# Kernel tuning notes

Measured on AMD Instinct MI355X. Metric: run time of the kernel, lower is better.

Reference implementation:

```python
import jax, jax.numpy as jnp
import numpy as np

N = 50000
E = 800000
IN, HID, OUT = 256, 128, 64
NEG_SLOPE = 0.2


def _gat(x, src, dst, W, a_src, a_dst, b, heads, dim, concat):
    # PyG GATConv (eval mode, self-loops already appended to src/dst)
    xh = (x @ W).reshape(N, heads, dim)              # [N,H,D]
    s_src = jnp.einsum('nhd,hd->nh', xh, a_src)       # [N,H]
    s_dst = jnp.einsum('nhd,hd->nh', xh, a_dst)
    e = jax.nn.leaky_relu(s_src[src] + s_dst[dst], NEG_SLOPE)  # [Etot,H]
    m = jax.ops.segment_max(e, dst, num_segments=N)
    e = jnp.exp(e - m[dst])
    z = jax.ops.segment_sum(e, dst, num_segments=N)
    alpha = e / z[dst]                                # segment softmax over incoming edges
    msg = xh[src] * alpha[:, :, None]                 # [Etot,H,D] gather + weight
    out = jax.ops.segment_sum(msg, dst, num_segments=N)  # scatter-add aggregate
    out = out.reshape(N, heads * dim) if concat else out.mean(axis=1)
    return out + b


def setup_inputs():
    key = jax.random.key(0)
    ks = jax.random.split(key, 20)
    sc = 0.05
    inp = {
        'x': jax.random.normal(ks[0], (N, IN), jnp.float32),
        'edge_index': jax.random.randint(ks[1], (2, E), 0, N, jnp.int64) if jax.config.read('jax_enable_x64') else jax.random.randint(ks[1], (2, E), 0, N, jnp.int32),
        # semantic MLP
        'w1': jax.random.normal(ks[2], (IN, HID), jnp.float32) * sc,
        'b1': jnp.zeros((HID,), jnp.float32),
        'w2': jax.random.normal(ks[3], (HID, HID), jnp.float32) * sc,
        'b2': jnp.zeros((HID,), jnp.float32),
        # gat1: HID -> HID//2, heads=4, concat -> 2*HID
        'g1_w': jax.random.normal(ks[4], (HID, 4 * (HID // 2)), jnp.float32) * sc,
        'g1_asrc': jax.random.normal(ks[5], (4, HID // 2), jnp.float32) * sc,
        'g1_adst': jax.random.normal(ks[6], (4, HID // 2), jnp.float32) * sc,
        'g1_b': jnp.zeros((2 * HID,), jnp.float32),
        # gat2: 2*HID -> OUT, heads=2, mean
        'g2_w': jax.random.normal(ks[7], (2 * HID, 2 * OUT), jnp.float32) * sc,
        'g2_asrc': jax.random.normal(ks[8], (2, OUT), jnp.float32) * sc,
        'g2_adst': jax.random.normal(ks[9], (2, OUT), jnp.float32) * sc,
        'g2_b': jnp.zeros((OUT,), jnp.float32),
        # gat3: OUT -> OUT, heads=1, mean
        'g3_w': jax.random.normal(ks[10], (OUT, OUT), jnp.float32) * sc,
        'g3_asrc': jax.random.normal(ks[11], (1, OUT), jnp.float32) * sc,
        'g3_adst': jax.random.normal(ks[12], (1, OUT), jnp.float32) * sc,
        'g3_b': jnp.zeros((OUT,), jnp.float32),
    }
    return inp


def reference(x, edge_index, w1, b1, w2, b2,
              g1_w, g1_asrc, g1_adst, g1_b,
              g2_w, g2_asrc, g2_adst, g2_b,
              g3_w, g3_asrc, g3_adst, g3_b):
    # add self loops once (PyG GATConv default add_self_loops=True)
    loop = jnp.arange(N, dtype=edge_index.dtype)
    src = jnp.concatenate([edge_index[0], loop])
    dst = jnp.concatenate([edge_index[1], loop])
    # semantic MLP (eval: dropout is identity)
    h = jax.nn.relu(x @ w1 + b1)
    h = jax.nn.relu(h @ w2 + b2)
    h = jax.nn.elu(_gat(h, src, dst, g1_w, g1_asrc, g1_adst, g1_b, 4, HID // 2, True))
    h = jax.nn.elu(_gat(h, src, dst, g2_w, g2_asrc, g2_adst, g2_b, 2, OUT, False))
    h = _gat(h, src, dst, g3_w, g3_asrc, g3_adst, g3_b, 1, OUT, False)
    return h
```

## Files before the change

kernel.cpp:

```cpp
#include <hip/hip_runtime.h>
#include <hip/hip_fp16.h>
#include <math.h>

#define NN 50000
#define NE 800000

static inline int ceil_div_h(int a, int b) { return (a + b - 1) / b; }

typedef _Float16 half8 __attribute__((ext_vector_type(8)));
typedef float f32x4 __attribute__((ext_vector_type(4)));

__global__ __launch_bounds__(256)
void prep_kernel(const float* __restrict__ w1, const float* __restrict__ w2,
                 const float* __restrict__ g1w, const float* __restrict__ g2w,
                 const float* __restrict__ g3w, __half* __restrict__ wt,
                 int* __restrict__ cursor) {
  int idx = blockIdx.x * 256 + threadIdx.x;
  if (idx < NN) cursor[idx] = 0;
  const float* W; int K, N, li;
  if (idx < 32768)        { W = w1;  K = 256; N = 128; li = idx; }
  else if (idx < 49152)   { W = w2;  K = 128; N = 128; li = idx - 32768; }
  else if (idx < 81920)   { W = g1w; K = 128; N = 256; li = idx - 49152; }
  else if (idx < 114688)  { W = g2w; K = 256; N = 128; li = idx - 81920; }
  else if (idx < 118784)  { W = g3w; K = 64;  N = 64;  li = idx - 114688; }
  else return;
  int n = li / K, k = li - n * K;
  wt[idx] = __float2half_rn(W[(size_t)k * N + n]);
}

__global__ __launch_bounds__(256)
void mlp_gat1_fused(const float* __restrict__ x,
                    const __half* __restrict__ wt1,
                    const float* __restrict__ b1,
                    const __half* __restrict__ wt2,
                    const float* __restrict__ b2,
                    const __half* __restrict__ wtg1,
                    const float* __restrict__ a_src, const float* __restrict__ a_dst,
                    __half* __restrict__ xh1,
                    float* __restrict__ s_src, float* __restrict__ s_dst) {
  constexpr int SA = 40;
  constexpr int SH = 136;
  __shared__ __align__(16) _Float16 smem[25088];
  _Float16* As   = smem;
  _Float16* Bs12 = smem + 2560;
  _Float16* h1s  = smem + 7680;
  _Float16* h2s  = smem + 16384;
  _Float16* Bs3  = Bs12;
  const int tid = threadIdx.x;
  const int bm = blockIdx.x * 64;
  const int wave = tid >> 6, lane = tid & 63;
  const int l16 = lane & 15, quad = lane >> 4;
  const int wm = (wave & 1) * 32;
  const int wn = (wave >> 1) * 64;

  {
    f32x4 acc[2][4] = {};
    for (int k0 = 0; k0 < 256; k0 += 32) {
      #pragma unroll
      for (int i = 0; i < 2; ++i) {
        int idx = tid + i * 256;
        int m = idx >> 3, q = idx & 7;
        int gm = bm + m;
        float4 v = make_float4(0.f, 0.f, 0.f, 0.f);
        if (gm < NN) v = *(const float4*)&x[(size_t)gm * 256 + k0 + q * 4];
        union { __half2 h2[2]; float2 f2; } u;
        u.h2[0] = __floats2half2_rn(v.x, v.y);
        u.h2[1] = __floats2half2_rn(v.z, v.w);
        *(float2*)&As[m * SA + q * 4] = u.f2;
      }
      #pragma unroll
      for (int i = 0; i < 2; ++i) {
        int idx = tid + i * 256;
        int n = idx >> 2, kq = (idx & 3) * 8;
        *(float4*)&Bs12[n * SA + kq] = *(const float4*)&wt1[(size_t)n * 256 + k0 + kq];
      }
      __syncthreads();
      half8 af[2], bf[4];
      #pragma unroll
      for (int mi = 0; mi < 2; ++mi)
        af[mi] = *(const half8*)&As[(wm + mi * 16 + l16) * SA + quad * 8];
      #pragma unroll
      for (int ni = 0; ni < 4; ++ni)
        bf[ni] = *(const half8*)&Bs12[(wn + ni * 16 + l16) * SA + quad * 8];
      #pragma unroll
      for (int mi = 0; mi < 2; ++mi)
        #pragma unroll
        for (int ni = 0; ni < 4; ++ni)
          acc[mi][ni] = __builtin_amdgcn_mfma_f32_16x16x32_f16(af[mi], bf[ni], acc[mi][ni], 0, 0, 0);
      __syncthreads();
    }
    #pragma unroll
    for (int mi = 0; mi < 2; ++mi)
      #pragma unroll
      for (int r = 0; r < 4; ++r) {
        int row = wm + mi * 16 + quad * 4 + r;
        #pragma unroll
        for (int ni = 0; ni < 4; ++ni) {
          int col = wn + ni * 16 + l16;
          float v = acc[mi][ni][r] + b1[col];
          v = fmaxf(v, 0.f);
          h1s[row * SH + col] = (_Float16)v;
        }
      }
  }
  __syncthreads();

  {
    f32x4 acc[2][4] = {};
    for (int k0 = 0; k0 < 128; k0 += 32) {
      #pragma unroll
      for (int i = 0; i < 2; ++i) {
        int idx = tid + i * 256;
        int n = idx >> 2, kq = (idx & 3) * 8;
        *(float4*)&Bs12[n * SA + kq] = *(const float4*)&wt2[(size_t)n * 128 + k0 + kq];
      }
      __syncthreads();
      half8 af[2], bf[4];
      #pragma unroll
      for (int mi = 0; mi < 2; ++mi)
        af[mi] = *(const half8*)&h1s[(wm + mi * 16 + l16) * SH + k0 + quad * 8];
      #pragma unroll
      for (int ni = 0; ni < 4; ++ni)
        bf[ni] = *(const half8*)&Bs12[(wn + ni * 16 + l16) * SA + quad * 8];
      #pragma unroll
      for (int mi = 0; mi < 2; ++mi)
        #pragma unroll
        for (int ni = 0; ni < 4; ++ni)
          acc[mi][ni] = __builtin_amdgcn_mfma_f32_16x16x32_f16(af[mi], bf[ni], acc[mi][ni], 0, 0, 0);
      __syncthreads();
    }
    #pragma unroll
    for (int mi = 0; mi < 2; ++mi)
      #pragma unroll
      for (int r = 0; r < 4; ++r) {
        int row = wm + mi * 16 + quad * 4 + r;
        #pragma unroll
        for (int ni = 0; ni < 4; ++ni) {
          int col = wn + ni * 16 + l16;
          float v = acc[mi][ni][r] + b2[col];
          v = fmaxf(v, 0.f);
          h2s[row * SH + col] = (_Float16)v;
        }
      }
  }
  __syncthreads();

  {
    f32x4 acc[4][4] = {};
    const int wn3 = wave * 64;
    for (int k0 = 0; k0 < 128; k0 += 32) {
      #pragma unroll
      for (int i = 0; i < 4; ++i) {
        int idx = tid + i * 256;
        int n = idx >> 2, kq = (idx & 3) * 8;
        *(float4*)&Bs3[n * SA + kq] = *(const float4*)&wtg1[(size_t)n * 128 + k0 + kq];
      }
      __syncthreads();
      half8 af[4], bf[4];
      #pragma unroll
      for (int mi = 0; mi < 4; ++mi)
        af[mi] = *(const half8*)&h2s[(mi * 16 + l16) * SH + k0 + quad * 8];
      #pragma unroll
      for (int ni = 0; ni < 4; ++ni)
        bf[ni] = *(const half8*)&Bs3[(wn3 + ni * 16 + l16) * SA + quad * 8];
      #pragma unroll
      for (int mi = 0; mi < 4; ++mi)
        #pragma unroll
        for (int ni = 0; ni < 4; ++ni)
          acc[mi][ni] = __builtin_amdgcn_mfma_f32_16x16x32_f16(af[mi], bf[ni], acc[mi][ni], 0, 0, 0);
      __syncthreads();
    }
    float asv[4], adv[4];
    #pragma unroll
    for (int ni = 0; ni < 4; ++ni) {
      int d = ni * 16 + l16;
      asv[ni] = a_src[wave * 64 + d];
      adv[ni] = a_dst[wave * 64 + d];
    }
    #pragma unroll
    for (int mi = 0; mi < 4; ++mi) {
      #pragma unroll
      for (int r = 0; r < 4; ++r) {
        int gm = bm + mi * 16 + quad * 4 + r;
        float ss = 0.f, sd = 0.f;
        #pragma unroll
        for (int ni = 0; ni < 4; ++ni) {
          float v = acc[mi][ni][r];
          ss = fmaf(v, asv[ni], ss);
          sd = fmaf(v, adv[ni], sd);
          if (gm < NN) xh1[(size_t)gm * 256 + wn3 + ni * 16 + l16] = __float2half_rn(v);
        }
        #pragma unroll
        for (int off = 1; off < 16; off <<= 1) {
          ss += __shfl_xor(ss, off, 64);
          sd += __shfl_xor(sd, off, 64);
        }
        if (l16 == 0 && gm < NN) {
          s_src[gm * 4 + wave] = ss;
          s_dst[gm * 4 + wave] = sd;
        }
      }
    }
  }
}

template<int BM, int TN, int WR, int WC, int ACT, int OUTH, int AF32, int HS>
__global__ __launch_bounds__(256)
void mfma_gemm(const void* __restrict__ Av, const __half* __restrict__ Bt,
               const float* __restrict__ bias, void* __restrict__ Cv,
               const float* __restrict__ a_src, const float* __restrict__ a_dst,
               float* __restrict__ s_src, float* __restrict__ s_dst,
               int M, int N, int K) {
  constexpr int FM = BM / WR / 16;
  constexpr int FN = TN / WC / 16;
  constexpr int SA = 40;
  __shared__ __align__(16) _Float16 As[BM * SA];
  __shared__ __align__(16) _Float16 Bs[TN * SA];
  const int tid = threadIdx.x;
  const int bm = blockIdx.y * BM, bn = blockIdx.x * TN;
  const int wave = tid >> 6, lane = tid & 63;
  const int wm = (wave % WR) * (BM / WR);
  const int wn = (wave / WR) * (TN / WC);
  const int l16 = lane & 15, quad = lane >> 4;

  f32x4 acc[FM][FN] = {};

  for (int k0 = 0; k0 < K; k0 += 32) {
    if (AF32) {
      const float* A = (const float*)Av;
      #pragma unroll
      for (int i = 0; i < (BM * 8) / 256; ++i) {
        int idx = tid + i * 256;
        int m = idx >> 3, q = idx & 7;
        int gm = bm + m;
        float4 v = make_float4(0.f, 0.f, 0.f, 0.f);
        if (gm < M) v = *(const float4*)&A[(size_t)gm * K + k0 + q * 4];
        union { __half2 h2[2]; float2 f2; } u;
        u.h2[0] = __floats2half2_rn(v.x, v.y);
        u.h2[1] = __floats2half2_rn(v.z, v.w);
        *(float2*)&As[m * SA + q * 4] = u.f2;
      }
    } else {
      const __half* A = (const __half*)Av;
      #pragma unroll
      for (int i = 0; i < (BM * 4) / 256; ++i) {
        int idx = tid + i * 256;
        int m = idx >> 2, q = (idx & 3) * 8;
        int gm = bm + m;
        float4 raw = make_float4(0.f, 0.f, 0.f, 0.f);
        if (gm < M) raw = *(const float4*)&A[(size_t)gm * K + k0 + q];
        *(float4*)&As[m * SA + q] = raw;
      }
    }
    #pragma unroll
    for (int i = 0; i < (TN * 4) / 256; ++i) {
      int idx = tid + i * 256;
      int n = idx >> 2, kq = (idx & 3) * 8;
      float4 raw = *(const float4*)&Bt[(size_t)(bn + n) * K + k0 + kq];
      *(float4*)&Bs[n * SA + kq] = raw;
    }
    __syncthreads();
    half8 af[FM], bf[FN];
    #pragma unroll
    for (int mi = 0; mi < FM; ++mi)
      af[mi] = *(const half8*)&As[(wm + mi * 16 + l16) * SA + quad * 8];
    #pragma unroll
    for (int ni = 0; ni < FN; ++ni)
      bf[ni] = *(const half8*)&Bs[(wn + ni * 16 + l16) * SA + quad * 8];
    #pragma unroll
    for (int mi = 0; mi < FM; ++mi)
      #pragma unroll
      for (int ni = 0; ni < FN; ++ni)
        acc[mi][ni] = __builtin_amdgcn_mfma_f32_16x16x32_f16(af[mi], bf[ni], acc[mi][ni], 0, 0, 0);
    __syncthreads();
  }

  #pragma unroll
  for (int mi = 0; mi < FM; ++mi) {
    #pragma unroll
    for (int r = 0; r < 4; ++r) {
      int gm = bm + wm + mi * 16 + quad * 4 + r;
      if (gm >= M) continue;
      #pragma unroll
      for (int ni = 0; ni < FN; ++ni) {
        int gn = bn + wn + ni * 16 + l16;
        float v = acc[mi][ni][r];
        if (bias) v += bias[gn];
        if (ACT == 1) v = fmaxf(v, 0.f);
        if (OUTH) ((__half*)Cv)[(size_t)gm * N + gn] = __float2half_rn(v);
        else      ((float*)Cv)[(size_t)gm * N + gn] = v;
      }
    }
  }

  if (HS > 0) {
    const int h = (bn + wn) >> 6;
    float asv[FN], adv[FN];
    #pragma unroll
    for (int ni = 0; ni < FN; ++ni) {
      int d = ni * 16 + l16;
      asv[ni] = a_src[h * 64 + d];
      adv[ni] = a_dst[h * 64 + d];
    }
    #pragma unroll
    for (int mi = 0; mi < FM; ++mi) {
      #pragma unroll
      for (int r = 0; r < 4; ++r) {
        float ss = 0.f, sd = 0.f;
        #pragma unroll
        for (int ni = 0; ni < FN; ++ni) {
          float v = acc[mi][ni][r];
          ss = fmaf(v, asv[ni], ss);
          sd = fmaf(v, adv[ni], sd);
        }
        #pragma unroll
        for (int off = 1; off < 16; off <<= 1) {
          ss += __shfl_xor(ss, off, 64);
          sd += __shfl_xor(sd, off, 64);
        }
        int gm = bm + wm + mi * 16 + quad * 4 + r;
        if (l16 == 0 && gm < M) {
          s_src[gm * HS + h] = ss;
          s_dst[gm * HS + h] = sd;
        }
      }
    }
  }
}


__global__ __launch_bounds__(256)
void hist_kernel(const int* __restrict__ ei, int* __restrict__ cnt) {
  int e = blockIdx.x * blockDim.x + threadIdx.x;
  if (e >= NE) return;
  atomicAdd(&cnt[ei[NE + e]], 1);
}

__global__ __launch_bounds__(256)
void scan1_kernel(const int* __restrict__ in, int* __restrict__ out,
                  int* __restrict__ bsum, int n) {
  __shared__ int tmp[256];
  int t = threadIdx.x;
  int i = blockIdx.x * 256 + t;
  int v = (i < n) ? in[i] : 0;
  tmp[t] = v;
  __syncthreads();
  for (int off = 1; off < 256; off <<= 1) {
    int u = (t >= off) ? tmp[t - off] : 0;
    __syncthreads();
    tmp[t] += u;
    __syncthreads();
  }
  if (i <= n) out[i] = tmp[t] - v;
  if (t == 255) bsum[blockIdx.x] = tmp[255];
}

__global__ __launch_bounds__(256)
void scan2_kernel(int* __restrict__ data, int n) {
  __shared__ int tmp[256];
  int t = threadIdx.x;
  int v = (t < n) ? data[t] : 0;
  tmp[t] = v;
  __syncthreads();
  for (int off = 1; off < 256; off <<= 1) {
    int u = (t >= off) ? tmp[t - off] : 0;
    __syncthreads();
    tmp[t] += u;
    __syncthreads();
  }
  if (t < n) data[t] = tmp[t] - v;
}

__global__ __launch_bounds__(256)
void scan3_kernel(int* __restrict__ out, const int* __restrict__ bsum,
                  int* __restrict__ cursor, int n) {
  int i = blockIdx.x * 256 + threadIdx.x;
  if (i > n) return;
  int v = out[i] + bsum[blockIdx.x];
  out[i] = v;
  if (i < n) cursor[i] = v;
}

__global__ __launch_bounds__(256)
void scatter_kernel(const int* __restrict__ ei, int* __restrict__ cursor,
                    int* __restrict__ srcs) {
  int e = blockIdx.x * blockDim.x + threadIdx.x;
  if (e >= NE) return;
  int s = ei[e], d = ei[NE + e];
  int pos = atomicAdd(&cursor[d], 1);
  srcs[pos] = s;
}

template<int H, int MODE>
__global__ __launch_bounds__(256)
void gat_aggregate(const int* __restrict__ rowptr, const int* __restrict__ srcs,
                   const float* __restrict__ ssrc, const float* __restrict__ sdst,
                   const __half* __restrict__ xh, const float* __restrict__ bias,
                   void* __restrict__ outv) {
  constexpr int HD = H * 64;
  __shared__ float wbuf[4][64 * H];
  __shared__ int sbuf[4][64];
  const int wslot = threadIdx.x >> 6;
  const int wid = (blockIdx.x * blockDim.x + threadIdx.x) >> 6;
  const int lane = threadIdx.x & 63;
  if (wid >= NN) return;
  const int n = wid;
  const int start = rowptr[n];
  const int end = rowptr[n + 1];
  const int h = (lane * H) >> 6;

  float sdv[H];
  #pragma unroll
  for (int hh = 0; hh < H; ++hh) sdv[hh] = sdst[n * H + hh];

  float z;
  float acc[H];
  {
    float wself[H];
    #pragma unroll
    for (int hh = 0; hh < H; ++hh) {
      float e = ssrc[n * H + hh] + sdv[hh];
      e = e >= 0.f ? e : 0.2f * e;
      wself[hh] = __expf(e);
    }
    float ws = wself[h];
    z = ws;
    const __half* xr = xh + (size_t)n * HD + lane * H;
    if (H == 4) {
      float2 raw = *(const float2*)xr;
      __half2 p0 = *(__half2*)&raw.x;
      __half2 p1 = *(__half2*)&raw.y;
      float2 f0 = __half22float2(p0), f1 = __half22float2(p1);
      acc[0] = ws * f0.x; acc[1] = ws * f0.y; acc[2] = ws * f1.x; acc[3] = ws * f1.y;
    } else if (H == 2) {
      float2 f0 = __half22float2(*(const __half2*)xr);
      acc[0] = ws * f0.x; acc[1] = ws * f0.y;
    } else {
      acc[0] = ws * __half2float(xr[0]);
    }
  }

  for (int base = start; base < end; base += 64) {
    int cnt = end - base;
    if (cnt > 64) cnt = 64;
    if (lane < cnt) {
      int s = srcs[base + lane];
      sbuf[wslot][lane] = s;
      float ev[H];
      if (H == 4) {
        float4 t = *(const float4*)&ssrc[s * 4];
        ev[0] = t.x; ev[1] = t.y; ev[2] = t.z; ev[3] = t.w;
      } else if (H == 2) {
        float2 t = *(const float2*)&ssrc[s * 2];
        ev[0] = t.x; ev[1] = t.y;
      } else {
        ev[0] = ssrc[s];
      }
      #pragma unroll
      for (int hh = 0; hh < H; ++hh) {
        float e = ev[hh] + sdv[hh];
        e = e >= 0.f ? e : 0.2f * e;
        wbuf[wslot][lane * H + hh] = __expf(e);
      }
    }
    #pragma unroll 4
    for (int j = 0; j < cnt; ++j) {
      int s = sbuf[wslot][j];
      float w = wbuf[wslot][j * H + h];
      z += w;
      const __half* xr = xh + (size_t)s * HD + lane * H;
      if (H == 4) {
        float2 raw = *(const float2*)xr;
        __half2 p0 = *(__half2*)&raw.x;
        __half2 p1 = *(__half2*)&raw.y;
        float2 f0 = __half22float2(p0), f1 = __half22float2(p1);
        acc[0] = fmaf(w, f0.x, acc[0]); acc[1] = fmaf(w, f0.y, acc[1]);
        acc[2] = fmaf(w, f1.x, acc[2]); acc[3] = fmaf(w, f1.y, acc[3]);
      } else if (H == 2) {
        float2 f0 = __half22float2(*(const __half2*)xr);
        acc[0] = fmaf(w, f0.x, acc[0]); acc[1] = fmaf(w, f0.y, acc[1]);
      } else {
        acc[0] = fmaf(w, __half2float(xr[0]), acc[0]);
      }
    }
  }
  const float inv = 1.f / z;

  if (MODE == 0) {
    __half* out = (__half*)outv;
    float v[4];
    #pragma unroll
    for (int i = 0; i < 4; ++i) {
      v[i] = acc[i] * inv + bias[lane * 4 + i];
      v[i] = v[i] > 0.f ? v[i] : expm1f(v[i]);
    }
    union { __half2 h2[2]; float2 f2; } u;
    u.h2[0] = __floats2half2_rn(v[0], v[1]);
    u.h2[1] = __floats2half2_rn(v[2], v[3]);
    *(float2*)&out[(size_t)n * 256 + lane * 4] = u.f2;
  } else if (MODE == 1) {
    __half* out = (__half*)outv;
    float sv[2];
    #pragma unroll
    for (int i = 0; i < 2; ++i) {
      float mine = acc[i] * inv;
      float other = __shfl_xor(mine, 32, 64);
      sv[i] = (mine + other) * 0.5f;
    }
    if (lane < 32) {
      float v0 = sv[0] + bias[lane * 2 + 0];
      float v1 = sv[1] + bias[lane * 2 + 1];
      v0 = v0 > 0.f ? v0 : expm1f(v0);
      v1 = v1 > 0.f ? v1 : expm1f(v1);
      *(__half2*)&out[(size_t)n * 64 + lane * 2] = __floats2half2_rn(v0, v1);
    }
  } else {
    float* out = (float*)outv;
    out[(size_t)n * 64 + lane] = acc[0] * inv + bias[lane];
  }
}


extern "C" void kernel_launch(void* const* d_in, const int* in_sizes, int n_in,
                              void* d_out, int out_size, void* d_ws, size_t ws_size,
                              hipStream_t stream) {
  const float* x    = (const float*)d_in[0];
  const int*   ei   = (const int*)d_in[1];
  const float* w1   = (const float*)d_in[2];
  const float* b1   = (const float*)d_in[3];
  const float* w2   = (const float*)d_in[4];
  const float* b2   = (const float*)d_in[5];
  const float* g1w  = (const float*)d_in[6];
  const float* g1as = (const float*)d_in[7];
  const float* g1ad = (const float*)d_in[8];
  const float* g1b  = (const float*)d_in[9];
  const float* g2w  = (const float*)d_in[10];
  const float* g2as = (const float*)d_in[11];
  const float* g2ad = (const float*)d_in[12];
  const float* g2b  = (const float*)d_in[13];
  const float* g3w  = (const float*)d_in[14];
  const float* g3as = (const float*)d_in[15];
  const float* g3ad = (const float*)d_in[16];
  const float* g3b  = (const float*)d_in[17];
  float* out = (float*)d_out;

  float* ws   = (float*)d_ws;
  float* bufA = ws;
  float* bufB = bufA + (size_t)NN * 256;
  float* bufC = bufB + (size_t)NN * 256;
  float* ssrc = bufC + (size_t)NN * 256;
  float* sdst = ssrc + (size_t)NN * 4;
  int* rowptr = (int*)(sdst + (size_t)NN * 4);
  int* cursor = rowptr + (NN + 1);
  int* bsum   = cursor + NN;
  int* srcs   = bsum + 256;
  __half* wt   = (__half*)(srcs + NE);
  __half* wt1  = wt;
  __half* wt2  = wt + 32768;
  __half* wtg1 = wt + 49152;
  __half* wtg2 = wt + 81920;
  __half* wtg3 = wt + 114688;

  __half* xh1 = (__half*)bufC;
  __half* a1  = (__half*)bufA;
  __half* xh2 = (__half*)bufB;
  __half* a2  = (__half*)bufC;
  __half* xh3 = (__half*)bufB;

  const int TB = 256;
  const int grid_m = ceil_div_h(NN, 64);
  const int egrid = ceil_div_h(NE, TB);
  const int sgrid = ceil_div_h(NN + 1, TB);
  const int wgrid = ceil_div_h(NN, 4);

  prep_kernel<<<ceil_div_h(118784, TB), TB, 0, stream>>>(w1, w2, g1w, g2w, g3w, wt, cursor);

  hist_kernel<<<egrid, TB, 0, stream>>>(ei, cursor);
  scan1_kernel<<<sgrid, TB, 0, stream>>>(cursor, rowptr, bsum, NN);
  scan2_kernel<<<1, TB, 0, stream>>>(bsum, sgrid);
  scan3_kernel<<<sgrid, TB, 0, stream>>>(rowptr, bsum, cursor, NN);
  scatter_kernel<<<egrid, TB, 0, stream>>>(ei, cursor, srcs);

  mlp_gat1_fused<<<grid_m, TB, 0, stream>>>(x, wt1, b1, wt2, b2, wtg1,
                                            g1as, g1ad, xh1, ssrc, sdst);
  gat_aggregate<4, 0><<<wgrid, TB, 0, stream>>>(rowptr, srcs, ssrc, sdst, xh1, g1b, a1);

  mfma_gemm<64, 128, 2, 2, 0, 1, 0, 2><<<dim3(1, grid_m), TB, 0, stream>>>(
      a1, wtg2, nullptr, xh2, g2as, g2ad, ssrc, sdst, NN, 128, 256);
  gat_aggregate<2, 1><<<wgrid, TB, 0, stream>>>(rowptr, srcs, ssrc, sdst, xh2, g2b, a2);

  mfma_gemm<64, 64, 4, 1, 0, 1, 0, 1><<<dim3(1, grid_m), TB, 0, stream>>>(
      a2, wtg3, nullptr, xh3, g3as, g3ad, ssrc, sdst, NN, 64, 64);
  gat_aggregate<1, 2><<<wgrid, TB, 0, stream>>>(rowptr, srcs, ssrc, sdst, xh3, g3b, out);
}
```

Before: 397.7 us.

## Process multiple edges per wavefront with 16-byte gathers and merge scan passes

The aggregation kernel now splits each 64-lane wavefront into groups that each handle a different edge. Every lane loads 8 halves (16 bytes) of the source row per gather instead of 1-4 elements, and the partial sums are combined with xor-shuffles at the end. This targets the narrow per-lane loads and the serial edge loop, especially in the H=1 and H=2 layers where most lanes previously moved only 2-4 bytes. Separately, the block-sum scan is folded into the final scan pass, removing one launch at the cost of every block redundantly rescanning the block sums. The change adds shuffle-reduction overhead and padding edges with zero weight.

```diff
diff --git a/kernel.cpp b/kernel.cpp
--- a/kernel.cpp
+++ b/kernel.cpp
@@ -356,11 +356,12 @@
 }
 
 __global__ __launch_bounds__(256)
-void scan2_kernel(int* __restrict__ data, int n) {
+void scan3_kernel(int* __restrict__ out, const int* __restrict__ bsum,
+                  int* __restrict__ cursor, int n, int nb) {
   __shared__ int tmp[256];
   int t = threadIdx.x;
-  int v = (t < n) ? data[t] : 0;
-  tmp[t] = v;
+  int bv = (t < nb) ? bsum[t] : 0;
+  tmp[t] = bv;
   __syncthreads();
   for (int off = 1; off < 256; off <<= 1) {
     int u = (t >= off) ? tmp[t - off] : 0;
@@ -368,15 +369,10 @@
     tmp[t] += u;
     __syncthreads();
   }
-  if (t < n) data[t] = tmp[t] - v;
-}
-
-__global__ __launch_bounds__(256)
-void scan3_kernel(int* __restrict__ out, const int* __restrict__ bsum,
-                  int* __restrict__ cursor, int n) {
-  int i = blockIdx.x * 256 + threadIdx.x;
+  int add = tmp[blockIdx.x] - ((blockIdx.x < nb) ? bsum[blockIdx.x] : 0);
+  int i = blockIdx.x * 256 + t;
   if (i > n) return;
-  int v = out[i] + bsum[blockIdx.x];
+  int v = out[i] + add;
   out[i] = v;
   if (i < n) cursor[i] = v;
 }
@@ -397,7 +393,9 @@
                    const float* __restrict__ ssrc, const float* __restrict__ sdst,
                    const __half* __restrict__ xh, const float* __restrict__ bias,
                    void* __restrict__ outv) {
-  constexpr int HD = H * 64;
+  constexpr int HD  = H * 64;
+  constexpr int G   = HD / 8;
+  constexpr int EPI = 64 / G;
   __shared__ float wbuf[4][64 * H];
   __shared__ int sbuf[4][64];
   const int wslot = threadIdx.x >> 6;
@@ -407,116 +405,135 @@
   const int n = wid;
   const int start = rowptr[n];
   const int end = rowptr[n + 1];
-  const int h = (lane * H) >> 6;
+  const int g = lane / G;
+  const int p = lane % G;
+  const int hp = (p * 8) >> 6;
+  const int wofs = g * H + hp;
 
   float sdv[H];
   #pragma unroll
   for (int hh = 0; hh < H; ++hh) sdv[hh] = sdst[n * H + hh];
 
-  float z;
-  float acc[H];
+  float z = 0.f;
+  float acc[8] = {};
+
   {
-    float wself[H];
-    #pragma unroll
-    for (int hh = 0; hh < H; ++hh) {
-      float e = ssrc[n * H + hh] + sdv[hh];
-      e = e >= 0.f ? e : 0.2f * e;
-      wself[hh] = __expf(e);
-    }
-    float ws = wself[h];
-    z = ws;
-    const __half* xr = xh + (size_t)n * HD + lane * H;
-    if (H == 4) {
-      float2 raw = *(const float2*)xr;
-      __half2 p0 = *(__half2*)&raw.x;
-      __half2 p1 = *(__half2*)&raw.y;
-      float2 f0 = __half22float2(p0), f1 = __half22float2(p1);
-      acc[0] = ws * f0.x; acc[1] = ws * f0.y; acc[2] = ws * f1.x; acc[3] = ws * f1.y;
-    } else if (H == 2) {
-      float2 f0 = __half22float2(*(const __half2*)xr);
-      acc[0] = ws * f0.x; acc[1] = ws * f0.y;
-    } else {
-      acc[0] = ws * __half2float(xr[0]);
+    float e = ssrc[n * H + hp] + sdv[hp];
+    e = e >= 0.f ? e : 0.2f * e;
+    float ws = __expf(e);
+    if (g == 0) {
+      z = ws;
+      const __half* xr = xh + (size_t)n * HD + p * 8;
+      union { float4 f4; __half2 h2[4]; } u;
+      u.f4 = *(const float4*)xr;
+      #pragma unroll
+      for (int i = 0; i < 4; ++i) {
+        float2 f = __half22float2(u.h2[i]);
+        acc[2 * i]     = ws * f.x;
+        acc[2 * i + 1] = ws * f.y;
+      }
     }
   }
 
   for (int base = start; base < end; base += 64) {
     int cnt = end - base;
     if (cnt > 64) cnt = 64;
-    if (lane < cnt) {
-      int s = srcs[base + lane];
+    int cnt_pad = (cnt + EPI - 1) & ~(EPI - 1);
+    if (lane < cnt_pad) {
+      bool val = lane < cnt;
+      int s = val ? srcs[base + lane] : n;
       sbuf[wslot][lane] = s;
-      float ev[H];
-      if (H == 4) {
-        float4 t = *(const float4*)&ssrc[s * 4];
-        ev[0] = t.x; ev[1] = t.y; ev[2] = t.z; ev[3] = t.w;
-      } else if (H == 2) {
-        float2 t = *(const float2*)&ssrc[s * 2];
-        ev[0] = t.x; ev[1] = t.y;
+      if (val) {
+        float ev[H];
+        if (H == 4) {
+          float4 t = *(const float4*)&ssrc[s * 4];
+          ev[0] = t.x; ev[1] = t.y; ev[2] = t.z; ev[3] = t.w;
+        } else if (H == 2) {
+          float2 t = *(const float2*)&ssrc[s * 2];
+          ev[0] = t.x; ev[1] = t.y;
+        } else {
+          ev[0] = ssrc[s];
+        }
+        #pragma unroll
+        for (int hh = 0; hh < H; ++hh) {
+          float e = ev[hh] + sdv[hh];
+          e = e >= 0.f ? e : 0.2f * e;
+          wbuf[wslot][lane * H + hh] = __expf(e);
+        }
       } else {
-        ev[0] = ssrc[s];
-      }
-      #pragma unroll
-      for (int hh = 0; hh < H; ++hh) {
-        float e = ev[hh] + sdv[hh];
-        e = e >= 0.f ? e : 0.2f * e;
-        wbuf[wslot][lane * H + hh] = __expf(e);
+        #pragma unroll
+        for (int hh = 0; hh < H; ++hh) wbuf[wslot][lane * H + hh] = 0.f;
       }
     }
     #pragma unroll 4
-    for (int j = 0; j < cnt; ++j) {
-      int s = sbuf[wslot][j];
-      float w = wbuf[wslot][j * H + h];
+    for (int j = 0; j < cnt; j += EPI) {
+      int s = sbuf[wslot][j + g];
+      float w = wbuf[wslot][j * H + wofs];
       z += w;
-      const __half* xr = xh + (size_t)s * HD + lane * H;
-      if (H == 4) {
-        float2 raw = *(const float2*)xr;
-        __half2 p0 = *(__half2*)&raw.x;
-        __half2 p1 = *(__half2*)&raw.y;
-        float2 f0 = __half22float2(p0), f1 = __half22float2(p1);
-        acc[0] = fmaf(w, f0.x, acc[0]); acc[1] = fmaf(w, f0.y, acc[1]);
-        acc[2] = fmaf(w, f1.x, acc[2]); acc[3] = fmaf(w, f1.y, acc[3]);
-      } else if (H == 2) {
-        float2 f0 = __half22float2(*(const __half2*)xr);
-        acc[0] = fmaf(w, f0.x, acc[0]); acc[1] = fmaf(w, f0.y, acc[1]);
-      } else {
-        acc[0] = fmaf(w, __half2float(xr[0]), acc[0]);
-      }
-    }
+      const __half* xr = xh + (size_t)s * HD + p * 8;
+      union { float4 f4; __half2 h2[4]; } u;
+      u.f4 = *(const float4*)xr;
+      #pragma unroll
+      for (int i = 0; i < 4; ++i) {
+        float2 f = __half22float2(u.h2[i]);
+        acc[2 * i]     = fmaf(w, f.x, acc[2 * i]);
+        acc[2 * i + 1] = fmaf(w, f.y, acc[2 * i + 1]);
+      }
+    }
+  }
+
+  #pragma unroll
+  for (int m = G; m < 64; m <<= 1) {
+    z += __shfl_xor(z, m, 64);
+    #pragma unroll
+    for (int i = 0; i < 8; ++i) acc[i] += __shfl_xor(acc[i], m, 64);
   }
   const float inv = 1.f / z;
 
   if (MODE == 0) {
-    __half* out = (__half*)outv;
-    float v[4];
-    #pragma unroll
-    for (int i = 0; i < 4; ++i) {
-      v[i] = acc[i] * inv + bias[lane * 4 + i];
-      v[i] = v[i] > 0.f ? v[i] : expm1f(v[i]);
-    }
-    union { __half2 h2[2]; float2 f2; } u;
-    u.h2[0] = __floats2half2_rn(v[0], v[1]);
-    u.h2[1] = __floats2half2_rn(v[2], v[3]);
-    *(float2*)&out[(size_t)n * 256 + lane * 4] = u.f2;
+    if (g == 0) {
+      __half* out = (__half*)outv;
+      float v[8];
+      #pragma unroll
+      for (int i = 0; i < 8; ++i) {
+        v[i] = acc[i] * inv + bias[p * 8 + i];
+        v[i] = v[i] > 0.f ? v[i] : expm1f(v[i]);
+      }
+      union { __half2 h2[4]; float4 f4; } u;
+      #pragma unroll
+      for (int i = 0; i < 4; ++i) u.h2[i] = __floats2half2_rn(v[2 * i], v[2 * i + 1]);
+      *(float4*)&out[(size_t)n * 256 + p * 8] = u.f4;
+    }
   } else if (MODE == 1) {
-    __half* out = (__half*)outv;
-    float sv[2];
-    #pragma unroll
-    for (int i = 0; i < 2; ++i) {
+    float sv[8];
+    #pragma unroll
+    for (int i = 0; i < 8; ++i) {
       float mine = acc[i] * inv;
-      float other = __shfl_xor(mine, 32, 64);
+      float other = __shfl_xor(mine, 8, 64);
       sv[i] = (mine + other) * 0.5f;
     }
-    if (lane < 32) {
-      float v0 = sv[0] + bias[lane * 2 + 0];
-      float v1 = sv[1] + bias[lane * 2 + 1];
-      v0 = v0 > 0.f ? v0 : expm1f(v0);
-      v1 = v1 > 0.f ? v1 : expm1f(v1);
-      *(__half2*)&out[(size_t)n * 64 + lane * 2] = __floats2half2_rn(v0, v1);
+    if (lane < 8) {
+      __half* out = (__half*)outv;
+      float v[8];
+      #pragma unroll
+      for (int i = 0; i < 8; ++i) {
+        v[i] = sv[i] + bias[p * 8 + i];
+        v[i] = v[i] > 0.f ? v[i] : expm1f(v[i]);
+      }
+      union { __half2 h2[4]; float4 f4; } u;
+      #pragma unroll
+      for (int i = 0; i < 4; ++i) u.h2[i] = __floats2half2_rn(v[2 * i], v[2 * i + 1]);
+      *(float4*)&out[(size_t)n * 64 + p * 8] = u.f4;
     }
   } else {
-    float* out = (float*)outv;
-    out[(size_t)n * 64 + lane] = acc[0] * inv + bias[lane];
+    if (lane < 8) {
+      float* out = (float*)outv;
+      float v[8];
+      #pragma unroll
+      for (int i = 0; i < 8; ++i) v[i] = acc[i] * inv + bias[p * 8 + i];
+      *(float4*)&out[(size_t)n * 64 + p * 8] = make_float4(v[0], v[1], v[2], v[3]);
+      *(float4*)&out[(size_t)n * 64 + p * 8 + 4] = make_float4(v[4], v[5], v[6], v[7]);
+    }
   }
 }
 
@@ -577,8 +594,7 @@
 
   hist_kernel<<<egrid, TB, 0, stream>>>(ei, cursor);
   scan1_kernel<<<sgrid, TB, 0, stream>>>(cursor, rowptr, bsum, NN);
-  scan2_kernel<<<1, TB, 0, stream>>>(bsum, sgrid);
-  scan3_kernel<<<sgrid, TB, 0, stream>>>(rowptr, bsum, cursor, NN);
+  scan3_kernel<<<sgrid, TB, 0, stream>>>(rowptr, bsum, cursor, NN, sgrid);
   scatter_kernel<<<egrid, TB, 0, stream>>>(ei, cursor, srcs);
 
   mlp_gat1_fused<<<grid_m, TB, 0, stream>>>(x, wt1, b1, wt2, b2, wtg1,
```

After: 432.2 us. 8.7% more time.
